# Optimization experiments

Hardware: AMD Instinct MI355X
Metric: run time of the kernel (lower is better)

Reference implementation:

```python
import jax, jax.numpy as jnp
import numpy as np

B, N, K = 1, 8192, 32
C_S, C_Z, C_H, H, PQ, PV = 384, 128, 16, 12, 4, 8
CZ4 = C_Z // 4
INF, EPS = 1e5, 1e-8
SOFTPLUS_INV_1 = 0.541324854612918


def _lin(key, i, o):
    return jax.random.normal(key, (i, o), jnp.float32) / np.sqrt(i)


def setup_inputs() -> dict:
    key = jax.random.key(0)
    ks = jax.random.split(key, 20)
    inp = {}
    inp["s"] = jax.random.normal(ks[0], (B, N, C_S), jnp.float32)
    inp["z"] = jax.random.normal(ks[1], (B, N, K, C_Z), jnp.float32)
    inp["edge_index"] = jax.random.randint(ks[2], (B, N, K), 0, N)
    m = jax.random.normal(ks[3], (B, N, 3, 3), jnp.float32)
    q, _ = jnp.linalg.qr(m)  # random orthonormal frames
    inp["rot"] = q
    inp["trans"] = 10.0 * jax.random.normal(ks[4], (B, N, 3), jnp.float32)
    inp["mask"] = jnp.ones((B, N), jnp.float32)
    hc = C_H * H
    inp["w_q"] = _lin(ks[5], C_S, hc); inp["b_q"] = jnp.zeros((hc,), jnp.float32)
    inp["w_kv"] = _lin(ks[6], C_S, 2 * hc); inp["b_kv"] = jnp.zeros((2 * hc,), jnp.float32)
    hpq = H * PQ * 3
    inp["w_qp"] = _lin(ks[7], C_S, hpq); inp["b_qp"] = jnp.zeros((hpq,), jnp.float32)
    hpkv = H * (PQ + PV) * 3
    inp["w_kvp"] = _lin(ks[8], C_S, hpkv); inp["b_kvp"] = jnp.zeros((hpkv,), jnp.float32)
    inp["w_b"] = _lin(ks[9], C_Z, H); inp["b_b"] = jnp.zeros((H,), jnp.float32)
    inp["w_dz"] = _lin(ks[10], C_Z, CZ4); inp["b_dz"] = jnp.zeros((CZ4,), jnp.float32)
    inp["head_weights"] = jnp.full((H,), SOFTPLUS_INV_1, jnp.float32)
    cat_dim = H * (CZ4 + C_H + PV * 4)
    inp["w_out"] = _lin(ks[11], cat_dim, C_S); inp["b_out"] = jnp.zeros((C_S,), jnp.float32)
    return inp


def reference(s, z, edge_index, rot, trans, mask,
              w_q, b_q, w_kv, b_kv, w_qp, b_qp, w_kvp, b_kvp,
              w_b, b_b, w_dz, b_dz, head_weights, w_out, b_out):
    gather = jax.vmap(lambda tab, idx: tab[idx])  # per-batch gather along N

    # scalar q/k/v
    q = (s @ w_q + b_q).reshape(B, N, H, C_H)
    kv = (s @ w_kv + b_kv).reshape(B, N, H, 2 * C_H)
    kv_g = gather(kv, edge_index)                      # [B,N,K,H,2C]
    k_g, v_g = kv_g[..., :C_H], kv_g[..., C_H:]

    # point q/k/v in global frame: layout is 3 stacked chunks (x,y,z)
    def to_pts(x):
        x = x.reshape(B, N, 3, -1).swapaxes(-1, -2)     # [B,N,H*P,3]
        return jnp.einsum('bnij,bnmj->bnmi', rot, x) + trans[:, :, None, :]

    q_pts = to_pts(s @ w_qp + b_qp).reshape(B, N, H, PQ, 3)
    kv_pts = to_pts(s @ w_kvp + b_kvp).reshape(B, N, H, PQ + PV, 3)
    kv_pts_g = gather(kv_pts, edge_index)               # [B,N,K,H,PQ+PV,3]
    k_pts_g, v_pts_g = kv_pts_g[..., :PQ, :], kv_pts_g[..., PQ:, :]

    # attention logits [B,H,N,K]
    a = jnp.einsum('bnhc,bnkhc->bhnk', q, k_g) * np.sqrt(1.0 / (3 * C_H))
    b_pair = z @ w_b + b_b                              # [B,N,K,H]
    a = a + np.sqrt(1.0 / 3) * jnp.transpose(b_pair, (0, 3, 1, 2))

    disp = q_pts[:, :, None] - k_pts_g                  # [B,N,K,H,PQ,3]
    pt_att = jnp.sum(disp * disp, axis=-1)              # [B,N,K,H,PQ]
    hw = jax.nn.softplus(head_weights) * np.sqrt(1.0 / (3 * (PQ * 9.0 / 2)))
    pt_att = -0.5 * jnp.sum(pt_att * hw[None, None, None, :, None], axis=-1)
    a = a + jnp.transpose(pt_att, (0, 3, 1, 2))

    edge_mask = gather(mask, edge_index)                # [B,N,K]
    a = a + (INF * (edge_mask - 1.0))[:, None]
    a = jax.nn.softmax(a, axis=-1)

    # outputs
    o = jnp.einsum('bhnk,bnkhc->bnhc', a, v_g).reshape(B, N, H * C_H)
    o_pt = jnp.einsum('bhnk,bnkhpx->bnhpx', a, v_pts_g)  # global frame
    o_pt = jnp.einsum('bnji,bnhpj->bnhpi', rot, o_pt - trans[:, :, None, None, :])
    o_pt_norm = jnp.sqrt(jnp.sum(o_pt * o_pt, axis=-1) + EPS).reshape(B, N, H * PV)
    o_pt = o_pt.reshape(B, N, H * PV, 3)

    pair_z = z @ w_dz + b_dz                            # [B,N,K,CZ4]
    o_pair = jnp.einsum('bhnk,bnkc->bnhc', a, pair_z).reshape(B, N, H * CZ4)

    cat = jnp.concatenate([o, o_pt[..., 0], o_pt[..., 1], o_pt[..., 2],
                           o_pt_norm, o_pair], axis=-1)
    return cat @ w_out + b_out
```

## Files before the change

### kernel.cpp

```cpp
#include <hip/hip_runtime.h>
#include <hip/hip_bf16.h>
#include <hip/hip_fp16.h>
#include <math.h>

#define N_NODES 8192
#define KNN 32

typedef unsigned short ushort_t;
typedef ushort_t ushort8 __attribute__((ext_vector_type(8)));
typedef ushort_t ushort4v __attribute__((ext_vector_type(4)));
typedef short short8v __attribute__((ext_vector_type(8)));
typedef float f32x4 __attribute__((ext_vector_type(4)));

static __device__ __forceinline__ float b2f(ushort_t u) {
    union { float f; unsigned int i; } v; v.i = ((unsigned int)u) << 16; return v.f;
}
static __device__ __forceinline__ ushort_t f2b(float f) {
    __hip_bfloat16 h = __float2bfloat16(f);
    return *(ushort_t*)&h;
}
static __device__ __forceinline__ float h2f(ushort_t u) {
    __half h = *(__half*)&u; return __half2float(h);
}
static __device__ __forceinline__ ushort_t f2h(float f) {
    __half h = __float2half(f); return *(ushort_t*)&h;
}

#define N_WALLT (1152 * 384)
#define N_WCATT (64 * 128)
#define N_WOUTT (384 * 960)
__global__ void build_weights(
    const float* __restrict__ wq,  const float* __restrict__ bq,
    const float* __restrict__ wkv, const float* __restrict__ bkv,
    const float* __restrict__ wqp, const float* __restrict__ bqp,
    const float* __restrict__ wkvp,const float* __restrict__ bkvp,
    const float* __restrict__ wb,  const float* __restrict__ bb,
    const float* __restrict__ wdz, const float* __restrict__ bdz,
    const float* __restrict__ wout,
    ushort_t* __restrict__ WallT, float* __restrict__ ball,
    ushort_t* __restrict__ WcatT, float* __restrict__ bcat,
    ushort_t* __restrict__ WoutT)
{
    int t = blockIdx.x * 256 + threadIdx.x;
    if (t < N_WALLT) {
        const int p = t / 384, k = t % 384;
        float v;
        if      (p < 192) v = wq  [k * 192 + p];
        else if (p < 576) v = wkv [k * 384 + (p - 192)];
        else if (p < 720) v = wqp [k * 144 + (p - 576)];
        else              v = wkvp[k * 432 + (p - 720)];
        WallT[t] = f2b(v);
    } else if (t < N_WALLT + N_WCATT) {
        const int u = t - N_WALLT;
        const int j = u >> 7, c = u & 127;
        float v = (j < 12) ? wb[c * 12 + j] : (j < 44 ? wdz[c * 32 + (j - 12)] : 0.0f);
        WcatT[u] = f2b(v);
    } else if (t < N_WALLT + N_WCATT + N_WOUTT) {
        const int u = t - N_WALLT - N_WCATT;
        const int p = u / 960, k = u % 960;
        WoutT[u] = f2b(wout[k * 384 + p]);
    } else {
        const int u = t - N_WALLT - N_WCATT - N_WOUTT;
        if (u < 1152) {
            float v;
            if      (u < 192)  v = bq[u];
            else if (u < 576)  v = bkv[u - 192];
            else if (u < 720)  v = bqp[u - 576];
            else               v = bkvp[u - 720];
            ball[u] = v;
        } else if (u < 1152 + 44) {
            const int w = u - 1152;
            bcat[w] = (w < 12) ? bb[w] : bdz[w - 12];
        }
    }
}
#define BW_TOTAL (N_WALLT + N_WCATT + N_WOUTT + 1152 + 44)

__global__ __launch_bounds__(256) void gemm_sproj(
    const float* __restrict__ A, const ushort_t* __restrict__ WT,
    const float* __restrict__ bias,
    ushort_t* __restrict__ qb, ushort_t* __restrict__ kbt,
    ushort_t* __restrict__ vbt, float* __restrict__ praw)
{
    __shared__ ushort_t As[128][40];
    __shared__ ushort_t Bs[128][40];

    const int tid  = threadIdx.x;
    const int ncol = 9;
    const int id   = blockIdx.x;
    const int xcd  = id & 7;
    const int qq   = id >> 3;
    const int row0 = ((qq / ncol) * 8 + xcd) * 128;
    const int col0 = (qq % ncol) * 128;
    const int K    = 384;

    const int wave = tid >> 6;
    const int lane = tid & 63;
    const int wm = (wave >> 1) * 64;
    const int wn = (wave & 1) * 64;
    const int m16 = lane & 15;
    const int kof = (lane >> 4) * 8;

    const int a_row = tid >> 1;
    const int a_kq  = (tid & 1) * 16;

    f32x4 acc[4][4];
#pragma unroll
    for (int i = 0; i < 4; ++i)
#pragma unroll
        for (int j = 0; j < 4; ++j) acc[i][j] = (f32x4)0.0f;

    for (int k0 = 0; k0 < K; k0 += 32) {
        {
            const float* ap = A + (size_t)(row0 + a_row) * K + (k0 + a_kq);
            float4 v0 = *(const float4*)(ap);
            float4 v1 = *(const float4*)(ap + 4);
            float4 v2 = *(const float4*)(ap + 8);
            float4 v3 = *(const float4*)(ap + 12);
            ushort8 u0, u1;
            u0[0] = f2b(v0.x); u0[1] = f2b(v0.y); u0[2] = f2b(v0.z); u0[3] = f2b(v0.w);
            u0[4] = f2b(v1.x); u0[5] = f2b(v1.y); u0[6] = f2b(v1.z); u0[7] = f2b(v1.w);
            u1[0] = f2b(v2.x); u1[1] = f2b(v2.y); u1[2] = f2b(v2.z); u1[3] = f2b(v2.w);
            u1[4] = f2b(v3.x); u1[5] = f2b(v3.y); u1[6] = f2b(v3.z); u1[7] = f2b(v3.w);
            *(ushort8*)&As[a_row][a_kq]     = u0;
            *(ushort8*)&As[a_row][a_kq + 8] = u1;
        }
        {
            const ushort_t* wp = WT + (size_t)(col0 + a_row) * K + (k0 + a_kq);
            *(ushort8*)&Bs[a_row][a_kq]     = *(const ushort8*)(wp);
            *(ushort8*)&Bs[a_row][a_kq + 8] = *(const ushort8*)(wp + 8);
        }
        __syncthreads();

        short8v a[4], b[4];
#pragma unroll
        for (int mb = 0; mb < 4; ++mb)
            a[mb] = *(const short8v*)&As[wm + mb * 16 + m16][kof];
#pragma unroll
        for (int nb = 0; nb < 4; ++nb)
            b[nb] = *(const short8v*)&Bs[wn + nb * 16 + m16][kof];
#pragma unroll
        for (int mb = 0; mb < 4; ++mb)
#pragma unroll
            for (int nb = 0; nb < 4; ++nb)
                acc[mb][nb] = __builtin_amdgcn_mfma_f32_16x16x32_bf16(
                    a[mb], b[nb], acc[mb][nb], 0, 0, 0);
        __syncthreads();
    }

    const int r_base = row0 + wm + (lane >> 4) * 4;
#pragma unroll
    for (int nb = 0; nb < 4; ++nb) {
        const int col = col0 + wn + nb * 16 + m16;
        const float bv = bias[col];
#pragma unroll
        for (int mb = 0; mb < 4; ++mb) {
#pragma unroll
            for (int r = 0; r < 4; ++r) {
                const int row = r_base + mb * 16 + r;
                const float v = acc[mb][nb][r] + bv;
                if (col < 192) {
                    qb[(size_t)row * 192 + col] = f2b(v);
                } else if (col < 576) {
                    const int u = col - 192, h = u >> 5, c = u & 31;
                    if (c < 16) kbt[(size_t)row * 192 + h * 16 + c] = f2b(v);
                    else        vbt[(size_t)row * 192 + h * 16 + (c - 16)] = f2b(v);
                } else {
                    praw[(size_t)row * 576 + (col - 576)] = v;
                }
            }
        }
    }
}

__global__ __launch_bounds__(256) void gemm_zproj(
    const float* __restrict__ Z, const ushort_t* __restrict__ WcT,
    const float* __restrict__ bc, ushort_t* __restrict__ zph)
{
    __shared__ ushort_t zt[64][136];
    __shared__ ushort_t wt[64][136];

    const int tid  = threadIdx.x;
    const int row0 = blockIdx.x * 64;
    const int wave = tid >> 6;
    const int lane = tid & 63;
    const int wm = (wave >> 1) * 32;
    const int wn = (wave & 1) * 32;
    const int m16 = lane & 15;
    const int kof = (lane >> 4) * 8;

    const int r  = tid >> 2;
    const int qt = (tid & 3) * 32;

    {
        const float* ap = Z + (size_t)(row0 + r) * 128 + qt;
#pragma unroll
        for (int i = 0; i < 4; ++i) {
            float4 v0 = *(const float4*)(ap + i * 8);
            float4 v1 = *(const float4*)(ap + i * 8 + 4);
            ushort8 u;
            u[0] = f2b(v0.x); u[1] = f2b(v0.y); u[2] = f2b(v0.z); u[3] = f2b(v0.w);
            u[4] = f2b(v1.x); u[5] = f2b(v1.y); u[6] = f2b(v1.z); u[7] = f2b(v1.w);
            *(ushort8*)&zt[r][qt + i * 8] = u;
        }
    }
    {
        const ushort_t* wp = WcT + (size_t)r * 128 + qt;
        *(ushort8*)&wt[r][qt]      = *(const ushort8*)(wp);
        *(ushort8*)&wt[r][qt + 8]  = *(const ushort8*)(wp + 8);
        *(ushort8*)&wt[r][qt + 16] = *(const ushort8*)(wp + 16);
        *(ushort8*)&wt[r][qt + 24] = *(const ushort8*)(wp + 24);
    }
    __syncthreads();

    f32x4 acc[2][2];
#pragma unroll
    for (int i = 0; i < 2; ++i)
#pragma unroll
        for (int j = 0; j < 2; ++j) acc[i][j] = (f32x4)0.0f;

#pragma unroll
    for (int ks = 0; ks < 4; ++ks) {
        short8v a[2], b[2];
        a[0] = *(const short8v*)&zt[wm + m16][ks * 32 + kof];
        a[1] = *(const short8v*)&zt[wm + 16 + m16][ks * 32 + kof];
        b[0] = *(const short8v*)&wt[wn + m16][ks * 32 + kof];
        b[1] = *(const short8v*)&wt[wn + 16 + m16][ks * 32 + kof];
#pragma unroll
        for (int mb = 0; mb < 2; ++mb)
#pragma unroll
            for (int nb = 0; nb < 2; ++nb)
                acc[mb][nb] = __builtin_amdgcn_mfma_f32_16x16x32_bf16(
                    a[mb], b[nb], acc[mb][nb], 0, 0, 0);
    }

    const int r_base = row0 + wm + (lane >> 4) * 4;
#pragma unroll
    for (int nb = 0; nb < 2; ++nb) {
        const int col = wn + nb * 16 + m16;
        if (col >= 44) continue;
        const float bv = bc[col];
#pragma unroll
        for (int mb = 0; mb < 2; ++mb) {
#pragma unroll
            for (int rr = 0; rr < 4; ++rr) {
                zph[(size_t)(r_base + mb * 16 + rr) * 48 + col] = f2b(acc[mb][nb][rr] + bv);
            }
        }
    }
}

__global__ __launch_bounds__(256) void gemm_out(
    const ushort_t* __restrict__ A, const ushort_t* __restrict__ WT,
    const float* __restrict__ bias, float* __restrict__ C)
{
    __shared__ ushort_t As[64][40];
    __shared__ ushort_t Bs[64][40];

    const int tid  = threadIdx.x;
    const int ncol = 6;
    const int id   = blockIdx.x;
    const int xcd  = id & 7;
    const int qq   = id >> 3;
    const int row0 = ((qq / ncol) * 8 + xcd) * 64;
    const int col0 = (qq % ncol) * 64;
    const int K = 960, P = 384;

    const int wave = tid >> 6;
    const int lane = tid & 63;
    const int wm = (wave >> 1) * 32;
    const int wn = (wave & 1) * 32;
    const int m16 = lane & 15;
    const int kof = (lane >> 4) * 8;

    const int a_row = tid >> 2;
    const int a_kq  = (tid & 3) * 8;

    f32x4 acc[2][2];
#pragma unroll
    for (int i = 0; i < 2; ++i)
#pragma unroll
        for (int j = 0; j < 2; ++j) acc[i][j] = (f32x4)0.0f;

    for (int k0 = 0; k0 < K; k0 += 32) {
        *(ushort8*)&As[a_row][a_kq] =
            *(const ushort8*)(A + (size_t)(row0 + a_row) * K + (k0 + a_kq));
        *(ushort8*)&Bs[a_row][a_kq] =
            *(const ushort8*)(WT + (size_t)(col0 + a_row) * K + (k0 + a_kq));
        __syncthreads();

        short8v a[2], b[2];
#pragma unroll
        for (int mb = 0; mb < 2; ++mb)
            a[mb] = *(const short8v*)&As[wm + mb * 16 + m16][kof];
#pragma unroll
        for (int nb = 0; nb < 2; ++nb)
            b[nb] = *(const short8v*)&Bs[wn + nb * 16 + m16][kof];
#pragma unroll
        for (int mb = 0; mb < 2; ++mb)
#pragma unroll
            for (int nb = 0; nb < 2; ++nb)
                acc[mb][nb] = __builtin_amdgcn_mfma_f32_16x16x32_bf16(
                    a[mb], b[nb], acc[mb][nb], 0, 0, 0);
        __syncthreads();
    }

    const int r_base = row0 + wm + (lane >> 4) * 4;
#pragma unroll
    for (int nb = 0; nb < 2; ++nb) {
        const int col = col0 + wn + nb * 16 + m16;
        const float bv = bias[col];
#pragma unroll
        for (int mb = 0; mb < 2; ++mb) {
#pragma unroll
            for (int r = 0; r < 4; ++r) {
                C[(size_t)(r_base + mb * 16 + r) * P + col] = acc[mb][nb][r] + bv;
            }
        }
    }
}

__global__ void prep_pts(const float* __restrict__ praw,
                         const float* __restrict__ rot,
                         const float* __restrict__ trans,
                         float* __restrict__ q_pts,
                         ushort_t* __restrict__ kpt,
                         ushort_t* __restrict__ vpt)
{
    int t = blockIdx.x * 256 + threadIdx.x;
    if (t >= N_NODES * 192) return;
    const int n = t / 192;
    const int m = t % 192;
    const float* row = praw + (size_t)n * 576;
    const float* R  = rot + n * 9;
    const float* tr = trans + n * 3;
    float X, Y, Z;
    if (m < 48) { X = row[m];       Y = row[48 + m];   Z = row[96 + m]; }
    else { const int pt = m - 48;
           X = row[144 + pt];  Y = row[288 + pt]; Z = row[432 + pt]; }
    const float gx = R[0] * X + R[1] * Y + R[2] * Z + tr[0];
    const float gy = R[3] * X + R[4] * Y + R[5] * Z + tr[1];
    const float gz = R[6] * X + R[7] * Y + R[8] * Z + tr[2];
    if (m < 48) {
        const int h = m >> 2, p = m & 3;
        float* dst = q_pts + (size_t)n * 144 + h * 12 + p * 3;
        dst[0] = gx; dst[1] = gy; dst[2] = gz;
    } else {
        const int pt = m - 48, h = pt / 12, p = pt % 12;
        if (p < 4) {
            ushort_t* dst = kpt + (size_t)n * 144 + h * 12 + p * 3;
            dst[0] = f2h(gx); dst[1] = f2h(gy); dst[2] = f2h(gz);
        } else {
            ushort_t* dst = vpt + (size_t)n * 288 + h * 24 + (p - 4) * 3;
            dst[0] = f2b(gx); dst[1] = f2b(gy); dst[2] = f2b(gz);
        }
    }
}

__global__ __launch_bounds__(256, 8) void attn_kernel(
    const ushort_t* __restrict__ qb,
    const ushort_t* __restrict__ kbt,
    const ushort_t* __restrict__ vbt,
    const float* __restrict__ q_pts,
    const ushort_t* __restrict__ kpt,
    const ushort_t* __restrict__ vpt,
    const ushort_t* __restrict__ zph,
    const int*   __restrict__ eidx,
    const float* __restrict__ mask,
    const float* __restrict__ rot,
    const float* __restrict__ trans,
    const float* __restrict__ head_weights,
    ushort_t* __restrict__ catb)
{
    const int n   = blockIdx.x;
    const int tid = threadIdx.x;

    __shared__ ushort_t zp[32][48];
    __shared__ float q_s[192];
    __shared__ float qp_s[144];
    __shared__ float a_s[12][33];
    __shared__ float opt[288];
    __shared__ int   idx_s[32];
    __shared__ float madd_s[32];
    __shared__ float R_s[9];
    __shared__ float t_s[3];
    __shared__ float hw_s[12];

    for (int i = tid; i < 192; i += 256) q_s[i]  = b2f(qb[(size_t)n * 192 + i]);
    for (int i = tid; i < 144; i += 256) qp_s[i] = q_pts[(size_t)n * 144 + i];
    if (tid < 32) {
        const int ix = eidx[n * 32 + tid];
        idx_s[tid]  = ix;
        madd_s[tid] = 100000.0f * (mask[ix] - 1.0f);
    }
    if (tid >= 32 && tid < 41) R_s[tid - 32]  = rot[n * 9 + (tid - 32)];
    if (tid >= 41 && tid < 44) t_s[tid - 41]  = trans[n * 3 + (tid - 41)];
    if (tid >= 44 && tid < 56) {
        float x = head_weights[tid - 44];
        hw_s[tid - 44] = log1pf(__expf(x)) * 0.13608276348795434f;
    }
    if (tid < 192) {
        const int r = tid / 6, sg = tid % 6;
        *(ushort8*)&zp[r][sg * 8] =
            *(const ushort8*)(zph + ((size_t)n * 32 + r) * 48 + sg * 8);
    }
    __syncthreads();

    for (int t = tid; t < 384; t += 256) {
        const int h = t >> 5, j = t & 31;
        const int ix = idx_s[j];
        const ushort_t* kr = kbt + (size_t)ix * 192 + h * 16;
        ushort8 k0 = *(const ushort8*)(kr);
        ushort8 k1 = *(const ushort8*)(kr + 8);
        const ushort_t* kpr = kpt + (size_t)ix * 144 + h * 12;
        ushort4v p0 = *(const ushort4v*)(kpr);
        ushort4v p1 = *(const ushort4v*)(kpr + 4);
        ushort4v p2 = *(const ushort4v*)(kpr + 8);

        const float* qh = q_s + h * 16;
        float dot = 0.0f;
#pragma unroll
        for (int c = 0; c < 8; ++c) dot += qh[c] * b2f(k0[c]);
#pragma unroll
        for (int c = 0; c < 8; ++c) dot += qh[8 + c] * b2f(k1[c]);

        const float* qp = qp_s + h * 12;
        float d, pt = 0.0f;
        d = qp[0]  - h2f(p0[0]); pt += d * d;  d = qp[1]  - h2f(p0[1]); pt += d * d;
        d = qp[2]  - h2f(p0[2]); pt += d * d;  d = qp[3]  - h2f(p0[3]); pt += d * d;
        d = qp[4]  - h2f(p1[0]); pt += d * d;  d = qp[5]  - h2f(p1[1]); pt += d * d;
        d = qp[6]  - h2f(p1[2]); pt += d * d;  d = qp[7]  - h2f(p1[3]); pt += d * d;
        d = qp[8]  - h2f(p2[0]); pt += d * d;  d = qp[9]  - h2f(p2[1]); pt += d * d;
        d = qp[10] - h2f(p2[2]); pt += d * d;  d = qp[11] - h2f(p2[3]); pt += d * d;

        a_s[h][j] = 0.14433756729740643f * dot
                  + 0.5773502691896258f * b2f(zp[j][h])
                  - 0.5f * hw_s[h] * pt
                  + madd_s[j];
    }
    __syncthreads();

    if (tid < 96) {
        const int h = tid >> 3, g = tid & 7;
        float a0 = a_s[h][g * 4 + 0], a1 = a_s[h][g * 4 + 1];
        float a2 = a_s[h][g * 4 + 2], a3 = a_s[h][g * 4 + 3];
        float m = fmaxf(fmaxf(a0, a1), fmaxf(a2, a3));
        m = fmaxf(m, __shfl_xor(m, 1)); m = fmaxf(m, __shfl_xor(m, 2));
        m = fmaxf(m, __shfl_xor(m, 4));
        float e0 = __expf(a0 - m), e1 = __expf(a1 - m);
        float e2 = __expf(a2 - m), e3 = __expf(a3 - m);
        float s = e0 + e1 + e2 + e3;
        s += __shfl_xor(s, 1); s += __shfl_xor(s, 2); s += __shfl_xor(s, 4);
        const float inv = 1.0f / s;
        a_s[h][g * 4 + 0] = e0 * inv; a_s[h][g * 4 + 1] = e1 * inv;
        a_s[h][g * 4 + 2] = e2 * inv; a_s[h][g * 4 + 3] = e3 * inv;
    }
    __syncthreads();

    ushort_t* catn = catb + (size_t)n * 960;
    if (tid < 48) {
        const int h = tid >> 2, cq = tid & 3;
        const ushort_t* base = vbt + h * 16 + cq * 4;
        float s0 = 0, s1 = 0, s2 = 0, s3 = 0;
#pragma unroll 8
        for (int j = 0; j < 32; ++j) {
            const int ix = idx_s[j];
            const float aj = a_s[h][j];
            ushort4v v = *(const ushort4v*)(base + (size_t)ix * 192);
            s0 += aj * b2f(v[0]); s1 += aj * b2f(v[1]);
            s2 += aj * b2f(v[2]); s3 += aj * b2f(v[3]);
        }
        ushort4v o = { f2b(s0), f2b(s1), f2b(s2), f2b(s3) };
        *(ushort4v*)&catn[h * 16 + cq * 4] = o;
    } else if (tid < 120) {
        const int u = tid - 48;
        const int h = u / 6, rq = u % 6;
        const ushort_t* base = vpt + h * 24 + rq * 4;
        float s0 = 0, s1 = 0, s2 = 0, s3 = 0;
#pragma unroll 8
        for (int j = 0; j < 32; ++j) {
            const int ix = idx_s[j];
            const float aj = a_s[h][j];
            ushort4v v = *(const ushort4v*)(base + (size_t)ix * 288);
            s0 += aj * b2f(v[0]); s1 += aj * b2f(v[1]);
            s2 += aj * b2f(v[2]); s3 += aj * b2f(v[3]);
        }
        float* od = opt + h * 24 + rq * 4;
        od[0] = s0; od[1] = s1; od[2] = s2; od[3] = s3;
    } else if (tid < 216) {
        const int u = tid - 120;
        const int h = u >> 3, cq = u & 7;
        float s0 = 0, s1 = 0, s2 = 0, s3 = 0;
#pragma unroll 8
        for (int j = 0; j < 32; ++j) {
            const float aj = a_s[h][j];
            ushort4v zv = *(const ushort4v*)&zp[j][12 + cq * 4];
            s0 += aj * b2f(zv[0]); s1 += aj * b2f(zv[1]);
            s2 += aj * b2f(zv[2]); s3 += aj * b2f(zv[3]);
        }
        ushort4v o = { f2b(s0), f2b(s1), f2b(s2), f2b(s3) };
        *(ushort4v*)&catn[576 + h * 32 + cq * 4] = o;
    }
    __syncthreads();

    if (tid < 96) {
        const int h = tid >> 3, p = tid & 7;
        const float* ob = opt + h * 24 + p * 3;
        float gx = ob[0] - t_s[0];
        float gy = ob[1] - t_s[1];
        float gz = ob[2] - t_s[2];
        float lx = R_s[0] * gx + R_s[3] * gy + R_s[6] * gz;
        float ly = R_s[1] * gx + R_s[4] * gy + R_s[7] * gz;
        float lz = R_s[2] * gx + R_s[5] * gy + R_s[8] * gz;
        const int hp = h * 8 + p;
        catn[192 + hp] = f2b(lx);
        catn[288 + hp] = f2b(ly);
        catn[384 + hp] = f2b(lz);
        catn[480 + hp] = f2b(sqrtf(lx * lx + ly * ly + lz * lz + 1e-8f));
    }
}

extern "C" void kernel_launch(void* const* d_in, const int* in_sizes, int n_in,
                              void* d_out, int out_size, void* d_ws, size_t ws_size,
                              hipStream_t stream)
{
    const float* s     = (const float*)d_in[0];
    const float* z     = (const float*)d_in[1];
    const int*   eidx  = (const int*)  d_in[2];
    const float* rot   = (const float*)d_in[3];
    const float* trans = (const float*)d_in[4];
    const float* mask  = (const float*)d_in[5];
    const float* w_q   = (const float*)d_in[6];
    const float* b_q   = (const float*)d_in[7];
    const float* w_kv  = (const float*)d_in[8];
    const float* b_kv  = (const float*)d_in[9];
    const float* w_qp  = (const float*)d_in[10];
    const float* b_qp  = (const float*)d_in[11];
    const float* w_kvp = (const float*)d_in[12];
    const float* b_kvp = (const float*)d_in[13];
    const float* w_b   = (const float*)d_in[14];
    const float* b_b   = (const float*)d_in[15];
    const float* w_dz  = (const float*)d_in[16];
    const float* b_dz  = (const float*)d_in[17];
    const float* hw    = (const float*)d_in[18];
    const float* w_out = (const float*)d_in[19];
    const float* b_out = (const float*)d_in[20];
    float* out = (float*)d_out;

    float* ws = (float*)d_ws;
    size_t off = 0;
    ushort_t* qb    = (ushort_t*)(ws + off); off += (size_t)N_NODES * 96;
    ushort_t* kbt   = (ushort_t*)(ws + off); off += (size_t)N_NODES * 96;
    ushort_t* vbt   = (ushort_t*)(ws + off); off += (size_t)N_NODES * 96;
    float* praw     = ws + off;              off += (size_t)N_NODES * 576;
    float* q_pts    = ws + off;              off += (size_t)N_NODES * 144;
    ushort_t* kpt   = (ushort_t*)(ws + off); off += (size_t)N_NODES * 72;
    ushort_t* vpt   = (ushort_t*)(ws + off); off += (size_t)N_NODES * 144;
    ushort_t* zph   = (ushort_t*)(ws + off); off += (size_t)N_NODES * KNN * 24;
    ushort_t* catb  = (ushort_t*)(ws + off); off += (size_t)N_NODES * 480;
    ushort_t* WallT = (ushort_t*)(ws + off); off += N_WALLT / 2;
    float* ball     = ws + off;              off += 1152;
    ushort_t* WcatT = (ushort_t*)(ws + off); off += N_WCATT / 2;
    float* bcat     = ws + off;              off += 44;
    ushort_t* WoutT = (ushort_t*)(ws + off); off += N_WOUTT / 2;

    build_weights<<<(BW_TOTAL + 255) / 256, 256, 0, stream>>>(
        w_q, b_q, w_kv, b_kv, w_qp, b_qp, w_kvp, b_kvp,
        w_b, b_b, w_dz, b_dz, w_out, WallT, ball, WcatT, bcat, WoutT);

    gemm_sproj<<<(N_NODES / 128) * 9, 256, 0, stream>>>(
        s, WallT, ball, qb, kbt, vbt, praw);

    gemm_zproj<<<(N_NODES * KNN) / 64, 256, 0, stream>>>(z, WcatT, bcat, zph);

    prep_pts<<<(N_NODES * 192 + 255) / 256, 256, 0, stream>>>(
        praw, rot, trans, q_pts, kpt, vpt);

    attn_kernel<<<N_NODES, 256, 0, stream>>>(
        qb, kbt, vbt, q_pts, kpt, vpt, zph, eidx, mask, rot, trans, hw, catb);

    gemm_out<<<(N_NODES / 64) * 6, 256, 0, stream>>>(catb, WoutT, b_out, out);
}
```

Baseline: 153.6 us.

## Process two nodes per attention block and store raw point projections in fp16

The attention kernel now handles two query nodes per 256-thread block, doubling the shared-memory arrays and looping thread work over both nodes. This cuts block count, raises lane utilisation in the phases that previously left most threads idle, and amortises the per-block setup. Separately, the intermediate point-projection buffer is stored as fp16 instead of fp32, halving its write and read traffic between the projection GEMM and prep_pts. The risk is some precision loss on the point coordinates before the frame transform, plus more shared memory per block, which may lower occupancy.

```diff
diff --git a/kernel.cpp b/kernel.cpp
--- a/kernel.cpp
+++ b/kernel.cpp
@@ -80,7 +80,7 @@
     const float* __restrict__ A, const ushort_t* __restrict__ WT,
     const float* __restrict__ bias,
     ushort_t* __restrict__ qb, ushort_t* __restrict__ kbt,
-    ushort_t* __restrict__ vbt, float* __restrict__ praw)
+    ushort_t* __restrict__ vbt, ushort_t* __restrict__ praw)
 {
     __shared__ ushort_t As[128][40];
     __shared__ ushort_t Bs[128][40];
@@ -166,7 +166,7 @@
                     if (c < 16) kbt[(size_t)row * 192 + h * 16 + c] = f2b(v);
                     else        vbt[(size_t)row * 192 + h * 16 + (c - 16)] = f2b(v);
                 } else {
-                    praw[(size_t)row * 576 + (col - 576)] = v;
+                    praw[(size_t)row * 576 + (col - 576)] = f2h(v);
                 }
             }
         }
@@ -320,7 +320,7 @@
     }
 }
 
-__global__ void prep_pts(const float* __restrict__ praw,
+__global__ void prep_pts(const ushort_t* __restrict__ praw,
                          const float* __restrict__ rot,
                          const float* __restrict__ trans,
                          float* __restrict__ q_pts,
@@ -331,13 +331,13 @@
     if (t >= N_NODES * 192) return;
     const int n = t / 192;
     const int m = t % 192;
-    const float* row = praw + (size_t)n * 576;
+    const ushort_t* row = praw + (size_t)n * 576;
     const float* R  = rot + n * 9;
     const float* tr = trans + n * 3;
     float X, Y, Z;
-    if (m < 48) { X = row[m];       Y = row[48 + m];   Z = row[96 + m]; }
+    if (m < 48) { X = h2f(row[m]);       Y = h2f(row[48 + m]);   Z = h2f(row[96 + m]); }
     else { const int pt = m - 48;
-           X = row[144 + pt];  Y = row[288 + pt]; Z = row[432 + pt]; }
+           X = h2f(row[144 + pt]);  Y = h2f(row[288 + pt]); Z = h2f(row[432 + pt]); }
     const float gx = R[0] * X + R[1] * Y + R[2] * Z + tr[0];
     const float gy = R[3] * X + R[4] * Y + R[5] * Z + tr[1];
     const float gz = R[6] * X + R[7] * Y + R[8] * Z + tr[2];
@@ -372,43 +372,58 @@
     const float* __restrict__ head_weights,
     ushort_t* __restrict__ catb)
 {
-    const int n   = blockIdx.x;
+    const int n0  = blockIdx.x * 2;
     const int tid = threadIdx.x;
 
-    __shared__ ushort_t zp[32][48];
-    __shared__ float q_s[192];
-    __shared__ float qp_s[144];
-    __shared__ float a_s[12][33];
-    __shared__ float opt[288];
-    __shared__ int   idx_s[32];
-    __shared__ float madd_s[32];
-    __shared__ float R_s[9];
-    __shared__ float t_s[3];
+    __shared__ ushort_t zp[2][32][48];
+    __shared__ float q_s[2][192];
+    __shared__ float qp_s[2][144];
+    __shared__ float a_s[2][12][33];
+    __shared__ float opt[2][288];
+    __shared__ int   idx_s[2][32];
+    __shared__ float madd_s[2][32];
+    __shared__ float R_s[2][9];
+    __shared__ float t_s[2][3];
     __shared__ float hw_s[12];
 
-    for (int i = tid; i < 192; i += 256) q_s[i]  = b2f(qb[(size_t)n * 192 + i]);
-    for (int i = tid; i < 144; i += 256) qp_s[i] = q_pts[(size_t)n * 144 + i];
-    if (tid < 32) {
-        const int ix = eidx[n * 32 + tid];
-        idx_s[tid]  = ix;
-        madd_s[tid] = 100000.0f * (mask[ix] - 1.0f);
-    }
-    if (tid >= 32 && tid < 41) R_s[tid - 32]  = rot[n * 9 + (tid - 32)];
-    if (tid >= 41 && tid < 44) t_s[tid - 41]  = trans[n * 3 + (tid - 41)];
-    if (tid >= 44 && tid < 56) {
-        float x = head_weights[tid - 44];
-        hw_s[tid - 44] = log1pf(__expf(x)) * 0.13608276348795434f;
-    }
-    if (tid < 192) {
-        const int r = tid / 6, sg = tid % 6;
-        *(ushort8*)&zp[r][sg * 8] =
-            *(const ushort8*)(zph + ((size_t)n * 32 + r) * 48 + sg * 8);
+    for (int i = tid; i < 384; i += 256) {
+        const int nl = i / 192, c = i % 192;
+        q_s[nl][c] = b2f(qb[(size_t)(n0 + nl) * 192 + c]);
+    }
+    for (int i = tid; i < 288; i += 256) {
+        const int nl = i / 144, c = i % 144;
+        qp_s[nl][c] = q_pts[(size_t)(n0 + nl) * 144 + c];
+    }
+    if (tid < 64) {
+        const int nl = tid >> 5, jj = tid & 31;
+        const int ix = eidx[(n0 + nl) * 32 + jj];
+        idx_s[nl][jj]  = ix;
+        madd_s[nl][jj] = 100000.0f * (mask[ix] - 1.0f);
+    }
+    if (tid >= 64 && tid < 82) {
+        const int nl = (tid - 64) / 9, e = (tid - 64) % 9;
+        R_s[nl][e] = rot[(n0 + nl) * 9 + e];
+    }
+    if (tid >= 82 && tid < 88) {
+        const int nl = (tid - 82) / 3, e = (tid - 82) % 3;
+        t_s[nl][e] = trans[(n0 + nl) * 3 + e];
+    }
+    if (tid >= 88 && tid < 100) {
+        float x = head_weights[tid - 88];
+        hw_s[tid - 88] = log1pf(__expf(x)) * 0.13608276348795434f;
+    }
+    for (int c = tid; c < 384; c += 256) {
+        const int nl = c / 192, cc = c % 192;
+        const int r = cc / 6, sg = cc % 6;
+        *(ushort8*)&zp[nl][r][sg * 8] =
+            *(const ushort8*)(zph + ((size_t)(n0 + nl) * 32 + r) * 48 + sg * 8);
     }
     __syncthreads();
 
-    for (int t = tid; t < 384; t += 256) {
-        const int h = t >> 5, j = t & 31;
-        const int ix = idx_s[j];
+    for (int t = tid; t < 768; t += 256) {
+        const int nl = t / 384, tt = t % 384;
+        const int h = tt >> 5, j = tt & 31;
+        const int ix = idx_s[nl][j];
         const ushort_t* kr = kbt + (size_t)ix * 192 + h * 16;
         ushort8 k0 = *(const ushort8*)(kr);
         ushort8 k1 = *(const ushort8*)(kr + 8);
@@ -417,14 +432,14 @@
         ushort4v p1 = *(const ushort4v*)(kpr + 4);
         ushort4v p2 = *(const ushort4v*)(kpr + 8);
 
-        const float* qh = q_s + h * 16;
+        const float* qh = q_s[nl] + h * 16;
         float dot = 0.0f;
 #pragma unroll
         for (int c = 0; c < 8; ++c) dot += qh[c] * b2f(k0[c]);
 #pragma unroll
         for (int c = 0; c < 8; ++c) dot += qh[8 + c] * b2f(k1[c]);
 
-        const float* qp = qp_s + h * 12;
+        const float* qp = qp_s[nl] + h * 12;
         float d, pt = 0.0f;
         d = qp[0]  - h2f(p0[0]); pt += d * d;  d = qp[1]  - h2f(p0[1]); pt += d * d;
         d = qp[2]  - h2f(p0[2]); pt += d * d;  d = qp[3]  - h2f(p0[3]); pt += d * d;
@@ -433,17 +448,18 @@
         d = qp[8]  - h2f(p2[0]); pt += d * d;  d = qp[9]  - h2f(p2[1]); pt += d * d;
         d = qp[10] - h2f(p2[2]); pt += d * d;  d = qp[11] - h2f(p2[3]); pt += d * d;
 
-        a_s[h][j] = 0.14433756729740643f * dot
-                  + 0.5773502691896258f * b2f(zp[j][h])
-                  - 0.5f * hw_s[h] * pt
-                  + madd_s[j];
+        a_s[nl][h][j] = 0.14433756729740643f * dot
+                      + 0.5773502691896258f * b2f(zp[nl][j][h])
+                      - 0.5f * hw_s[h] * pt
+                      + madd_s[nl][j];
     }
     __syncthreads();
 
-    if (tid < 96) {
-        const int h = tid >> 3, g = tid & 7;
-        float a0 = a_s[h][g * 4 + 0], a1 = a_s[h][g * 4 + 1];
-        float a2 = a_s[h][g * 4 + 2], a3 = a_s[h][g * 4 + 3];
+    if (tid < 192) {
+        const int nl = tid / 96, u = tid % 96;
+        const int h = u >> 3, g = u & 7;
+        float a0 = a_s[nl][h][g * 4 + 0], a1 = a_s[nl][h][g * 4 + 1];
+        float a2 = a_s[nl][h][g * 4 + 2], a3 = a_s[nl][h][g * 4 + 3];
         float m = fmaxf(fmaxf(a0, a1), fmaxf(a2, a3));
         m = fmaxf(m, __shfl_xor(m, 1)); m = fmaxf(m, __shfl_xor(m, 2));
         m = fmaxf(m, __shfl_xor(m, 4));
@@ -452,66 +468,71 @@
         float s = e0 + e1 + e2 + e3;
         s += __shfl_xor(s, 1); s += __shfl_xor(s, 2); s += __shfl_xor(s, 4);
         const float inv = 1.0f / s;
-        a_s[h][g * 4 + 0] = e0 * inv; a_s[h][g * 4 + 1] = e1 * inv;
-        a_s[h][g * 4 + 2] = e2 * inv; a_s[h][g * 4 + 3] = e3 * inv;
+        a_s[nl][h][g * 4 + 0] = e0 * inv; a_s[nl][h][g * 4 + 1] = e1 * inv;
+        a_s[nl][h][g * 4 + 2] = e2 * inv; a_s[nl][h][g * 4 + 3] = e3 * inv;
     }
     __syncthreads();
 
-    ushort_t* catn = catb + (size_t)n * 960;
-    if (tid < 48) {
-        const int h = tid >> 2, cq = tid & 3;
-        const ushort_t* base = vbt + h * 16 + cq * 4;
-        float s0 = 0, s1 = 0, s2 = 0, s3 = 0;
+    for (int t = tid; t < 432; t += 256) {
+        const int nl = t / 216, k = t % 216;
+        ushort_t* catn = catb + (size_t)(n0 + nl) * 960;
+        if (k < 48) {
+            const int h = k >> 2, cq = k & 3;
+            const ushort_t* base = vbt + h * 16 + cq * 4;
+            float s0 = 0, s1 = 0, s2 = 0, s3 = 0;
 #pragma unroll 8
-        for (int j = 0; j < 32; ++j) {
-            const int ix = idx_s[j];
-            const float aj = a_s[h][j];
-            ushort4v v = *(const ushort4v*)(base + (size_t)ix * 192);
-            s0 += aj * b2f(v[0]); s1 += aj * b2f(v[1]);
-            s2 += aj * b2f(v[2]); s3 += aj * b2f(v[3]);
-        }
-        ushort4v o = { f2b(s0), f2b(s1), f2b(s2), f2b(s3) };
-        *(ushort4v*)&catn[h * 16 + cq * 4] = o;
-    } else if (tid < 120) {
-        const int u = tid - 48;
-        const int h = u / 6, rq = u % 6;
-        const ushort_t* base = vpt + h * 24 + rq * 4;
-        float s0 = 0, s1 = 0, s2 = 0, s3 = 0;
+            for (int j = 0; j < 32; ++j) {
+                const int ix = idx_s[nl][j];
+                const float aj = a_s[nl][h][j];
+                ushort4v v = *(const ushort4v*)(base + (size_t)ix * 192);
+                s0 += aj * b2f(v[0]); s1 += aj * b2f(v[1]);
+                s2 += aj * b2f(v[2]); s3 += aj * b2f(v[3]);
+            }
+            ushort4v o = { f2b(s0), f2b(s1), f2b(s2), f2b(s3) };
+            *(ushort4v*)&catn[h * 16 + cq * 4] = o;
+        } else if (k < 120) {
+            const int u = k - 48;
+            const int h = u / 6, rq = u % 6;
+            const ushort_t* base = vpt + h * 24 + rq * 4;
+            float s0 = 0, s1 = 0, s2 = 0, s3 = 0;
 #pragma unroll 8
-        for (int j = 0; j < 32; ++j) {
-            const int ix = idx_s[j];
-            const float aj = a_s[h][j];
-            ushort4v v = *(const ushort4v*)(base + (size_t)ix * 288);
-            s0 += aj * b2f(v[0]); s1 += aj * b2f(v[1]);
-            s2 += aj * b2f(v[2]); s3 += aj * b2f(v[3]);
-        }
-        float* od = opt + h * 24 + rq * 4;
-        od[0] = s0; od[1] = s1; od[2] = s2; od[3] = s3;
-    } else if (tid < 216) {
-        const int u = tid - 120;
-        const int h = u >> 3, cq = u & 7;
-        float s0 = 0, s1 = 0, s2 = 0, s3 = 0;
+            for (int j = 0; j < 32; ++j) {
+                const int ix = idx_s[nl][j];
+                const float aj = a_s[nl][h][j];
+                ushort4v v = *(const ushort4v*)(base + (size_t)ix * 288);
+                s0 += aj * b2f(v[0]); s1 += aj * b2f(v[1]);
+                s2 += aj * b2f(v[2]); s3 += aj * b2f(v[3]);
+            }
+            float* od = opt[nl] + h * 24 + rq * 4;
+            od[0] = s0; od[1] = s1; od[2] = s2; od[3] = s3;
+        } else {
+            const int u = k - 120;
+            const int h = u >> 3, cq = u & 7;
+            float s0 = 0, s1 = 0, s2 = 0, s3 = 0;
 #pragma unroll 8
-        for (int j = 0; j < 32; ++j) {
-            const float aj = a_s[h][j];
-            ushort4v zv = *(const ushort4v*)&zp[j][12 + cq * 4];
-            s0 += aj * b2f(zv[0]); s1 += aj * b2f(zv[1]);
-            s2 += aj * b2f(zv[2]); s3 += aj * b2f(zv[3]);
-        }
-        ushort4v o = { f2b(s0), f2b(s1), f2b(s2), f2b(s3) };
-        *(ushort4v*)&catn[576 + h * 32 + cq * 4] = o;
+            for (int j = 0; j < 32; ++j) {
+                const float aj = a_s[nl][h][j];
+                ushort4v zv = *(const ushort4v*)&zp[nl][j][12 + cq * 4];
+                s0 += aj * b2f(zv[0]); s1 += aj * b2f(zv[1]);
+                s2 += aj * b2f(zv[2]); s3 += aj * b2f(zv[3]);
+            }
+            ushort4v o = { f2b(s0), f2b(s1), f2b(s2), f2b(s3) };
+            *(ushort4v*)&catn[576 + h * 32 + cq * 4] = o;
+        }
     }
     __syncthreads();
 
-    if (tid < 96) {
-        const int h = tid >> 3, p = tid & 7;
-        const float* ob = opt + h * 24 + p * 3;
-        float gx = ob[0] - t_s[0];
-        float gy = ob[1] - t_s[1];
-        float gz = ob[2] - t_s[2];
-        float lx = R_s[0] * gx + R_s[3] * gy + R_s[6] * gz;
-        float ly = R_s[1] * gx + R_s[4] * gy + R_s[7] * gz;
-        float lz = R_s[2] * gx + R_s[5] * gy + R_s[8] * gz;
+    if (tid < 192) {
+        const int nl = tid / 96, u = tid % 96;
+        const int h = u >> 3, p = u & 7;
+        ushort_t* catn = catb + (size_t)(n0 + nl) * 960;
+        const float* ob = opt[nl] + h * 24 + p * 3;
+        float gx = ob[0] - t_s[nl][0];
+        float gy = ob[1] - t_s[nl][1];
+        float gz = ob[2] - t_s[nl][2];
+        float lx = R_s[nl][0] * gx + R_s[nl][3] * gy + R_s[nl][6] * gz;
+        float ly = R_s[nl][1] * gx + R_s[nl][4] * gy + R_s[nl][7] * gz;
+        float lz = R_s[nl][2] * gx + R_s[nl][5] * gy + R_s[nl][8] * gz;
         const int hp = h * 8 + p;
         catn[192 + hp] = f2b(lx);
         catn[288 + hp] = f2b(ly);
@@ -552,7 +573,7 @@
     ushort_t* qb    = (ushort_t*)(ws + off); off += (size_t)N_NODES * 96;
     ushort_t* kbt   = (ushort_t*)(ws + off); off += (size_t)N_NODES * 96;
     ushort_t* vbt   = (ushort_t*)(ws + off); off += (size_t)N_NODES * 96;
-    float* praw     = ws + off;              off += (size_t)N_NODES * 576;
+    ushort_t* praw  = (ushort_t*)(ws + off); off += (size_t)N_NODES * 288;
     float* q_pts    = ws + off;              off += (size_t)N_NODES * 144;
     ushort_t* kpt   = (ushort_t*)(ws + off); off += (size_t)N_NODES * 72;
     ushort_t* vpt   = (ushort_t*)(ws + off); off += (size_t)N_NODES * 144;
@@ -576,7 +597,7 @@
     prep_pts<<<(N_NODES * 192 + 255) / 256, 256, 0, stream>>>(
         praw, rot, trans, q_pts, kpt, vpt);
 
-    attn_kernel<<<N_NODES, 256, 0, stream>>>(
+    attn_kernel<<<N_NODES / 2, 256, 0, stream>>>(
         qb, kbt, vbt, q_pts, kpt, vpt, zph, eidx, mask, rot, trans, hw, catb);
 
     gemm_out<<<(N_NODES / 64) * 6, 256, 0, stream>>>(catb, WoutT, b_out, out);
```

Result: slower. 157.3 us (+2.4%).
